# Optimization experiments

Hardware: AMD Instinct MI355X
Metric: run time of the kernel (lower is better)

## Reference

```python
import jax, jax.numpy as jnp
import numpy as np

N = 50000      # total nodes in batch
E = 800000     # edges (before self-loops)
F_IN = 64      # num_node_features
HID = 64       # hidden_channels
H = 4          # heads (hidden layers)
G = 512        # number of graphs
NEG_SLOPE = 0.2


def setup_inputs() -> dict:
    key = jax.random.key(0)
    ks = jax.random.split(key, 12)
    x = jax.random.normal(ks[0], (N, F_IN), dtype=jnp.float32)
    edge_index = jax.random.randint(ks[1], (2, E), 0, N, dtype=jnp.int32)
    # deterministic sorted graph assignment: all G segments non-empty
    batch = ((jnp.arange(N) * G) // N).astype(jnp.int32)

    def w(k, shape, fan_in):
        return (jax.random.normal(k, shape, jnp.float32) / np.sqrt(fan_in)).astype(jnp.float32)

    return {
        "x": x, "edge_index": edge_index, "batch": batch,
        # layer 0: in=F_IN, heads=4, concat -> out 256
        "W0": w(ks[2], (F_IN, H * HID), F_IN),
        "att_src0": w(ks[3], (H, HID), HID), "att_dst0": w(ks[4], (H, HID), HID),
        "b0": jnp.zeros((H * HID,), jnp.float32),
        # layer 1: in=256, heads=4, concat -> out 256
        "W1": w(ks[5], (H * HID, H * HID), H * HID),
        "att_src1": w(ks[6], (H, HID), HID), "att_dst1": w(ks[7], (H, HID), HID),
        "b1": jnp.zeros((H * HID,), jnp.float32),
        # layer 2: in=256, heads=1, concat=False -> out 64
        "W2": w(ks[8], (H * HID, 1 * HID), H * HID),
        "att_src2": w(ks[9], (1, HID), HID), "att_dst2": w(ks[10], (1, HID), HID),
        "b2": jnp.zeros((HID,), jnp.float32),
    }


def gat_layer(x, src, dst, W, att_src, att_dst, bias, concat):
    # PyG GATConv (eval mode, add_self_loops already applied to src/dst)
    n = x.shape[0]
    h, c = att_src.shape
    z = (x @ W).reshape(n, h, c)                       # [N,H,C]
    a_s = jnp.sum(z * att_src, axis=-1)                # [N,H]
    a_d = jnp.sum(z * att_dst, axis=-1)                # [N,H]
    e = jax.nn.leaky_relu(a_s[src] + a_d[dst], NEG_SLOPE)   # [E',H]
    # segment softmax over incoming edges of each target node
    e_max = jax.ops.segment_max(e, dst, num_segments=n)
    e_exp = jnp.exp(e - e_max[dst])
    denom = jax.ops.segment_sum(e_exp, dst, num_segments=n)
    alpha = e_exp / (denom[dst] + 1e-16)               # [E',H]
    msg = z[src] * alpha[:, :, None]                   # [E',H,C]
    out = jax.ops.segment_sum(msg, dst, num_segments=n)  # [N,H,C]
    out = out.reshape(n, h * c) if concat else out.mean(axis=1)
    return out + bias


def reference(x, edge_index, batch, W0, att_src0, att_dst0, b0,
              W1, att_src1, att_dst1, b1, W2, att_src2, att_dst2, b2):
    n = x.shape[0]
    loops = jnp.arange(n, dtype=edge_index.dtype)
    src = jnp.concatenate([edge_index[0], loops])
    dst = jnp.concatenate([edge_index[1], loops])
    h = gat_layer(x, src, dst, W0, att_src0, att_dst0, b0, concat=True)
    h = jax.nn.elu(h)
    h = gat_layer(h, src, dst, W1, att_src1, att_dst1, b1, concat=True)
    h = jax.nn.elu(h)
    h = gat_layer(h, src, dst, W2, att_src2, att_dst2, b2, concat=False)
    # global max pool over nodes of each graph -> [G, HID]
    return jax.ops.segment_max(h, batch, num_segments=G)
```

## Files before the change

### kernel.cpp

```cpp
#include <hip/hip_runtime.h>
#include <math.h>


typedef __attribute__((ext_vector_type(8))) short short8v;
typedef __attribute__((ext_vector_type(16))) float f32x16;

__device__ __forceinline__ float lrelu(float x) { return x > 0.f ? x : 0.2f * x; }

__device__ __forceinline__ unsigned short f2bf(float x) {
    unsigned u = __float_as_uint(x);
    return (unsigned short)((u + 0x7FFFu + ((u >> 16) & 1u)) >> 16);
}
__device__ __forceinline__ float bf2f(unsigned short h) {
    return __uint_as_float(((unsigned)h) << 16);
}
__device__ __forceinline__ float readlane_f(float v, int l) {
    return __uint_as_float((unsigned)__builtin_amdgcn_readlane((int)__float_as_uint(v), l));
}

__global__ void k_count(const int* __restrict__ dst, int E, int* __restrict__ deg) {
    int e = blockIdx.x * 256 + threadIdx.x;
    if (e < E) atomicAdd(&deg[dst[e]], 1);
}

__global__ __launch_bounds__(256) void k_scan1(const int* __restrict__ deg,
                                               int* __restrict__ incl,
                                               int* __restrict__ bsum, int N) {
    const int i = blockIdx.x * 256 + threadIdx.x;
    const int lane = threadIdx.x & 63;
    const int wv = threadIdx.x >> 6;
    int sc = (i < N) ? deg[i] + 1 : 0;
#pragma unroll
    for (int off = 1; off < 64; off <<= 1) {
        int t = __shfl_up(sc, off, 64);
        if (lane >= off) sc += t;
    }
    __shared__ int wsum[4];
    if (lane == 63) wsum[wv] = sc;
    __syncthreads();
    int woff = 0;
#pragma unroll
    for (int k = 0; k < 3; k++)
        if (wv > k) woff += wsum[k];
    sc += woff;
    if (i < N) incl[i] = sc;
    if (threadIdx.x == 255) bsum[blockIdx.x] = sc;
}

__global__ __launch_bounds__(1024) void k_scan2(int* __restrict__ bsum, int nb) {
    const int t = threadIdx.x;
    const int lane = t & 63;
    const int wv = t >> 6;
    int sc = (t < nb) ? bsum[t] : 0;
#pragma unroll
    for (int off = 1; off < 64; off <<= 1) {
        int u = __shfl_up(sc, off, 64);
        if (lane >= off) sc += u;
    }
    __shared__ int wsum[16];
    if (lane == 63) wsum[wv] = sc;
    __syncthreads();
    int woff = 0;
#pragma unroll
    for (int k = 0; k < 15; k++)
        if (wv > k) woff += wsum[k];
    sc += woff;
    if (t < nb) bsum[t] = sc;
}

__global__ void k_scan3(const int* __restrict__ deg, const int* __restrict__ incl,
                        const int* __restrict__ bsum, int* __restrict__ rowptr,
                        int* __restrict__ cursor, int N, int nb) {
    int i = blockIdx.x * 256 + threadIdx.x;
    if (i < N) {
        const int off = (blockIdx.x > 0) ? bsum[blockIdx.x - 1] : 0;
        const int excl = incl[i] + off - (deg[i] + 1);
        rowptr[i] = excl;
        cursor[i] = excl;
        if (i == N - 1) rowptr[N] = bsum[nb - 1];
    }
}

__global__ void k_scatter(const int* __restrict__ src, const int* __restrict__ dst, int E,
                          int N, int* __restrict__ cursor, int* __restrict__ col) {
    int e = blockIdx.x * 256 + threadIdx.x;
    if (e < E) {
        int d = dst[e];
        int p = atomicAdd(&cursor[d], 1);
        col[p] = src[e];
    } else if (e < E + N) {
        int n = e - E;
        int p = atomicAdd(&cursor[n], 1);
        col[p] = n;
    }
}

__global__ void k_setup(const float* __restrict__ W0, const float* __restrict__ W1,
                        const float* __restrict__ W2, const float* __restrict__ as0,
                        const float* __restrict__ ad0,
                        unsigned short* __restrict__ wt0h, unsigned short* __restrict__ wt0l,
                        unsigned short* __restrict__ wt1h, unsigned short* __restrict__ wt1l,
                        unsigned short* __restrict__ wt2h, unsigned short* __restrict__ wt2l,
                        float* __restrict__ vs0, float* __restrict__ vd0) {
    const int b = blockIdx.x;
    const int t = threadIdx.x;
    if (b < 64) {
        const int i = b * 256 + t;
        const int c = i / 64, k = i % 64;
        const float xw = W0[(size_t)k * 256 + c];
        const unsigned short h = f2bf(xw);
        wt0h[i] = h;
        wt0l[i] = f2bf(xw - bf2f(h));
    } else if (b < 320) {
        const int i = (b - 64) * 256 + t;
        const int c = i / 256, k = i % 256;
        const float xw = W1[(size_t)k * 256 + c];
        const unsigned short h = f2bf(xw);
        wt1h[i] = h;
        wt1l[i] = f2bf(xw - bf2f(h));
    } else if (b < 384) {
        const int i = (b - 320) * 256 + t;
        const int c = i / 256, k = i % 256;
        const float xw = W2[(size_t)k * 64 + c];
        const unsigned short h = f2bf(xw);
        wt2h[i] = h;
        wt2l[i] = f2bf(xw - bf2f(h));
    } else {
        const int k = t;
        if (k < 64) {
            for (int h = 0; h < 4; h++) {
                float s = 0.f, d = 0.f;
                for (int c = 0; c < 64; c++) {
                    float w = W0[(size_t)k * 256 + h * 64 + c];
                    s = fmaf(w, as0[h * 64 + c], s);
                    d = fmaf(w, ad0[h * 64 + c], d);
                }
                vs0[h * 64 + k] = s;
                vd0[h * 64 + k] = d;
            }
        }
    }
}

__global__ __launch_bounds__(256) void k_att0(
    const float* __restrict__ X, const float* __restrict__ vs, const float* __restrict__ vd,
    float* __restrict__ As, float* __restrict__ Ad, unsigned short* __restrict__ xb, int N) {
    const int n = blockIdx.x * 4 + (threadIdx.x >> 6);
    const int lane = threadIdx.x & 63;
    if (n >= N) return;
    const float xv = X[(size_t)n * 64 + lane];
    xb[(size_t)n * 64 + lane] = f2bf(xv);
#pragma unroll
    for (int h = 0; h < 4; h++) {
        float ps = xv * vs[h * 64 + lane];
        float pd = xv * vd[h * 64 + lane];
#pragma unroll
        for (int off = 1; off < 64; off <<= 1) {
            ps += __shfl_xor(ps, off, 64);
            pd += __shfl_xor(pd, off, 64);
        }
        if (lane == 0) {
            As[(size_t)n * 4 + h] = ps;
            Ad[(size_t)n * 4 + h] = pd;
        }
    }
}

__global__ __launch_bounds__(256) void k_aggx(
    const unsigned short* __restrict__ Xb, const float* __restrict__ As,
    const float* __restrict__ Ad, const int* __restrict__ rowptr,
    const int* __restrict__ col, unsigned short* __restrict__ ohi,
    unsigned short* __restrict__ olo, int N) {
    __shared__ float wlds[4][64][4];
    const int wv = threadIdx.x >> 6;
    const int n = blockIdx.x * 4 + wv;
    const int lane = threadIdx.x & 63;
    if (n >= N) return;

    const int start = rowptr[n];
    const int total = rowptr[n + 1] - start;
    const int* __restrict__ cp = col + start;
    const float4 adn = *reinterpret_cast<const float4*>(Ad + (size_t)n * 4);

    float a0 = 0.f, a1 = 0.f, a2 = 0.f, a3 = 0.f;
    float4 dv = make_float4(0.f, 0.f, 0.f, 0.f);

    for (int base = 0; base < total; base += 64) {
        const int cnt = min(64, total - base);
        const int i = base + lane;
        int s = 0;
        float4 w = make_float4(0.f, 0.f, 0.f, 0.f);
        if (i < total) {
            s = cp[i];
            const float4 av = *reinterpret_cast<const float4*>(As + (size_t)s * 4);
            w.x = __expf(lrelu(av.x + adn.x));
            w.y = __expf(lrelu(av.y + adn.y));
            w.z = __expf(lrelu(av.z + adn.z));
            w.w = __expf(lrelu(av.w + adn.w));
        }
        dv.x += w.x; dv.y += w.y; dv.z += w.z; dv.w += w.w;
        *reinterpret_cast<float4*>(&wlds[wv][lane][0]) = w;

        int jj = 0;
        for (; jj + 4 <= cnt; jj += 4) {
            int sb[4];
            float4 wj[4];
            float xv[4];
#pragma unroll
            for (int u = 0; u < 4; u++) {
                sb[u] = __builtin_amdgcn_readlane(s, jj + u);
                wj[u] = *reinterpret_cast<const float4*>(&wlds[wv][jj + u][0]);
            }
#pragma unroll
            for (int u = 0; u < 4; u++) xv[u] = bf2f(Xb[(size_t)sb[u] * 64 + lane]);
#pragma unroll
            for (int u = 0; u < 4; u++) {
                a0 = fmaf(wj[u].x, xv[u], a0);
                a1 = fmaf(wj[u].y, xv[u], a1);
                a2 = fmaf(wj[u].z, xv[u], a2);
                a3 = fmaf(wj[u].w, xv[u], a3);
            }
        }
        for (; jj < cnt; jj++) {
            const int s0 = __builtin_amdgcn_readlane(s, jj);
            const float4 wj = *reinterpret_cast<const float4*>(&wlds[wv][jj][0]);
            const float xv = bf2f(Xb[(size_t)s0 * 64 + lane]);
            a0 = fmaf(wj.x, xv, a0);
            a1 = fmaf(wj.y, xv, a1);
            a2 = fmaf(wj.z, xv, a2);
            a3 = fmaf(wj.w, xv, a3);
        }
    }

#pragma unroll
    for (int off = 1; off < 64; off <<= 1) {
        dv.x += __shfl_xor(dv.x, off, 64);
        dv.y += __shfl_xor(dv.y, off, 64);
        dv.z += __shfl_xor(dv.z, off, 64);
        dv.w += __shfl_xor(dv.w, off, 64);
    }

    const float o[4] = {a0 / (dv.x + 1e-16f), a1 / (dv.y + 1e-16f),
                        a2 / (dv.z + 1e-16f), a3 / (dv.w + 1e-16f)};
#pragma unroll
    for (int h = 0; h < 4; h++) {
        const unsigned short hb = f2bf(o[h]);
        ohi[(size_t)n * 256 + h * 64 + lane] = hb;
        olo[(size_t)n * 256 + h * 64 + lane] = f2bf(o[h] - bf2f(hb));
    }
}

__global__ __launch_bounds__(256) void k_gemm_pe(
    const unsigned short* __restrict__ Ahi, const unsigned short* __restrict__ Alo,
    const unsigned short* __restrict__ Bhi, const unsigned short* __restrict__ Blo,
    const float* __restrict__ bias, unsigned short* __restrict__ Ohi, int N) {
    constexpr int LD = 40, BM = 128, K = 64;
    __shared__ unsigned short sa[2][BM * LD];
    __shared__ unsigned short sb[2][64 * LD];

    const int tid = threadIdx.x;
    const int n0 = blockIdx.x * BM;
    const int hh = blockIdx.y;
    const int wid = tid >> 6, lane = tid & 63;

    const unsigned short* __restrict__ Ah = Ahi + hh * 64;
    const unsigned short* __restrict__ Al = Alo + hh * 64;
    const unsigned short* __restrict__ Bh = Bhi + hh * 64 * K;
    const unsigned short* __restrict__ Bl = Blo + hh * 64 * K;

    f32x16 acc[2];
#pragma unroll
    for (int n = 0; n < 2; n++)
#pragma unroll
        for (int i = 0; i < 16; i++) acc[n][i] = 0.f;

    const int srow = tid >> 2, schk = tid & 3;

    for (int kb = 0; kb < K; kb += 32) {
        __syncthreads();
#pragma unroll
        for (int rr = 0; rr < 2; rr++) {
            const int r = srow + rr * 64;
            const int row = n0 + r;
            short8v vh = {0, 0, 0, 0, 0, 0, 0, 0}, vl = {0, 0, 0, 0, 0, 0, 0, 0};
            if (row < N) {
                vh = *reinterpret_cast<const short8v*>(Ah + (size_t)row * 256 + kb + schk * 8);
                vl = *reinterpret_cast<const short8v*>(Al + (size_t)row * 256 + kb + schk * 8);
            }
            *reinterpret_cast<short8v*>(&sa[0][r * LD + schk * 8]) = vh;
            *reinterpret_cast<short8v*>(&sa[1][r * LD + schk * 8]) = vl;
        }
        {
            const short8v vh =
                *reinterpret_cast<const short8v*>(Bh + (size_t)srow * K + kb + schk * 8);
            const short8v vl =
                *reinterpret_cast<const short8v*>(Bl + (size_t)srow * K + kb + schk * 8);
            *reinterpret_cast<short8v*>(&sb[0][srow * LD + schk * 8]) = vh;
            *reinterpret_cast<short8v*>(&sb[1][srow * LD + schk * 8]) = vl;
        }
        __syncthreads();
#pragma unroll
        for (int ks = 0; ks < 2; ks++) {
            const int koff = ks * 16 + (lane >> 5) * 8;
            const int ar = wid * 32 + (lane & 31);
            const short8v ah = *reinterpret_cast<const short8v*>(&sa[0][ar * LD + koff]);
            const short8v al = *reinterpret_cast<const short8v*>(&sa[1][ar * LD + koff]);
            short8v bh[2], bl[2];
#pragma unroll
            for (int n = 0; n < 2; n++) {
                const int br = n * 32 + (lane & 31);
                bh[n] = *reinterpret_cast<const short8v*>(&sb[0][br * LD + koff]);
                bl[n] = *reinterpret_cast<const short8v*>(&sb[1][br * LD + koff]);
            }
#pragma unroll
            for (int n = 0; n < 2; n++) {
                acc[n] = __builtin_amdgcn_mfma_f32_32x32x16_bf16(ah, bh[n], acc[n], 0, 0, 0);
                acc[n] = __builtin_amdgcn_mfma_f32_32x32x16_bf16(ah, bl[n], acc[n], 0, 0, 0);
                acc[n] = __builtin_amdgcn_mfma_f32_32x32x16_bf16(al, bh[n], acc[n], 0, 0, 0);
            }
        }
    }

    const int rowb = n0 + wid * 32 + 4 * (lane >> 5);
#pragma unroll
    for (int n = 0; n < 2; n++) {
        const int c = (lane & 31) + n * 32;
        const float bv = bias[hh * 64 + c];
#pragma unroll
        for (int r = 0; r < 16; r++) {
            const int row = rowb + (r & 3) + 8 * (r >> 2);
            if (row < N) {
                float ov = acc[n][r] + bv;
                ov = (ov > 0.f) ? ov : expm1f(ov);
                Ohi[(size_t)row * 256 + hh * 64 + c] = f2bf(ov);
            }
        }
    }
}

template <int K, int COLS, int BM, int BN, int WN, int OUTMODE>
__global__ __launch_bounds__(256) void k_gemm_z(
    const unsigned short* __restrict__ Ahi,
    const unsigned short* __restrict__ Bhi, const unsigned short* __restrict__ Blo,
    const float* __restrict__ att_src, const float* __restrict__ att_dst,
    unsigned short* __restrict__ Zb, unsigned char* __restrict__ Zq,
    float* __restrict__ scq, float* __restrict__ As, float* __restrict__ Ad, int N) {
    constexpr int LD = 40;
    constexpr int WAVES_N = BN / WN;
    constexpr int WAVES_M = 4 / WAVES_N;
    constexpr int WM = BM / WAVES_M;
    constexpr int MW = WM / 32, NW = WN / 32;
    constexpr int H = COLS / 64;
    __shared__ unsigned short sa[BM * LD];
    __shared__ unsigned short sb[2][BN * LD];

    const int tid = threadIdx.x;
    const int n0 = blockIdx.x * BM;
    const int c0 = blockIdx.y * BN;
    const int wid = tid >> 6, lane = tid & 63;
    const int wr = wid / WAVES_N, wc = wid % WAVES_N;

    f32x16 acc[MW][NW];
#pragma unroll
    for (int m = 0; m < MW; m++)
#pragma unroll
        for (int n = 0; n < NW; n++)
#pragma unroll
            for (int i = 0; i < 16; i++) acc[m][n][i] = 0.f;

    const int srow = tid >> 2, schk = tid & 3;

    for (int kb = 0; kb < K; kb += 32) {
        __syncthreads();
#pragma unroll
        for (int rr = 0; rr < BM / 64; rr++) {
            const int r = srow + rr * 64;
            const int row = n0 + r;
            short8v vh = {0, 0, 0, 0, 0, 0, 0, 0};
            if (row < N)
                vh = *reinterpret_cast<const short8v*>(Ahi + (size_t)row * K + kb + schk * 8);
            *reinterpret_cast<short8v*>(&sa[r * LD + schk * 8]) = vh;
        }
#pragma unroll
        for (int rr = 0; rr < BN / 64; rr++) {
            const int cc = srow + rr * 64;
            const short8v vh =
                *reinterpret_cast<const short8v*>(Bhi + (size_t)(c0 + cc) * K + kb + schk * 8);
            const short8v vl =
                *reinterpret_cast<const short8v*>(Blo + (size_t)(c0 + cc) * K + kb + schk * 8);
            *reinterpret_cast<short8v*>(&sb[0][cc * LD + schk * 8]) = vh;
            *reinterpret_cast<short8v*>(&sb[1][cc * LD + schk * 8]) = vl;
        }
        __syncthreads();
#pragma unroll
        for (int ks = 0; ks < 2; ks++) {
            const int koff = ks * 16 + (lane >> 5) * 8;
            short8v ah[MW], bh[NW], bl[NW];
#pragma unroll
            for (int m = 0; m < MW; m++) {
                const int ar = wr * WM + m * 32 + (lane & 31);
                ah[m] = *reinterpret_cast<const short8v*>(&sa[ar * LD + koff]);
            }
#pragma unroll
            for (int n = 0; n < NW; n++) {
                const int br = wc * WN + n * 32 + (lane & 31);
                bh[n] = *reinterpret_cast<const short8v*>(&sb[0][br * LD + koff]);
                bl[n] = *reinterpret_cast<const short8v*>(&sb[1][br * LD + koff]);
            }
#pragma unroll
            for (int m = 0; m < MW; m++)
#pragma unroll
                for (int n = 0; n < NW; n++) {
                    acc[m][n] = __builtin_amdgcn_mfma_f32_32x32x16_bf16(ah[m], bh[n], acc[m][n], 0, 0, 0);
                    acc[m][n] = __builtin_amdgcn_mfma_f32_32x32x16_bf16(ah[m], bl[n], acc[m][n], 0, 0, 0);
                }
        }
    }

    const int colb = c0 + wc * WN + (lane & 31);
    const int rowb = n0 + wr * WM + 4 * (lane >> 5);

    if constexpr (OUTMODE == 0) {
#pragma unroll
        for (int m = 0; m < MW; m++)
#pragma unroll
            for (int n = 0; n < NW; n++)
#pragma unroll
                for (int r = 0; r < 16; r++) {
                    const int row = rowb + m * 32 + (r & 3) + 8 * (r >> 2);
                    if (row < N) Zb[(size_t)row * COLS + colb + n * 32] = f2bf(acc[m][n][r]);
                }
    } else {
        float lmax = 0.f;
#pragma unroll
        for (int m = 0; m < MW; m++)
#pragma unroll
            for (int n = 0; n < NW; n++)
#pragma unroll
                for (int r = 0; r < 16; r++) lmax = fmaxf(lmax, fabsf(acc[m][n][r]));
#pragma unroll
        for (int off = 1; off < 64; off <<= 1) lmax = fmaxf(lmax, __shfl_xor(lmax, off, 64));
        __shared__ float smax[4];
        if (lane == 0) smax[wid] = lmax;
        __syncthreads();
        const float qmax = fmaxf(fmaxf(smax[wc], smax[wc + 2]), 1e-20f);
        const float sc = qmax * (1.f / 127.f);
        const float rsc = 127.f / qmax;
        if (lane == 0 && wr == 0) scq[blockIdx.x * 4 + blockIdx.y * 2 + wc] = sc;
#pragma unroll
        for (int m = 0; m < MW; m++)
#pragma unroll
            for (int n = 0; n < NW; n++)
#pragma unroll
                for (int r = 0; r < 16; r++) {
                    const int row = rowb + m * 32 + (r & 3) + 8 * (r >> 2);
                    if (row < N) {
                        int q = __float2int_rn(acc[m][n][r] * rsc) + 128;
                        q = min(255, max(0, q));
                        Zq[(size_t)row * COLS + colb + n * 32] = (unsigned char)q;
                    }
                }
    }

    const int hh = (c0 + wc * WN) >> 6;
    float asv[NW], adv[NW];
#pragma unroll
    for (int n = 0; n < NW; n++) {
        asv[n] = att_src[colb + n * 32];
        adv[n] = att_dst[colb + n * 32];
    }
#pragma unroll
    for (int m = 0; m < MW; m++)
#pragma unroll
        for (int r = 0; r < 16; r++) {
            const int row = rowb + m * 32 + (r & 3) + 8 * (r >> 2);
            float ps = 0.f, pd = 0.f;
#pragma unroll
            for (int n = 0; n < NW; n++) {
                ps = fmaf(acc[m][n][r], asv[n], ps);
                pd = fmaf(acc[m][n][r], adv[n], pd);
            }
#pragma unroll
            for (int off = 1; off < 32; off <<= 1) {
                ps += __shfl_xor(ps, off, 64);
                pd += __shfl_xor(pd, off, 64);
            }
            if ((lane & 31) == 0 && row < N) {
                As[(size_t)row * H + hh] = ps;
                Ad[(size_t)row * H + hh] = pd;
            }
        }
}

__device__ __forceinline__ unsigned fenc(float f) {
    unsigned u = __float_as_uint(f);
    return (u & 0x80000000u) ? ~u : (u | 0x80000000u);
}

__global__ __launch_bounds__(256) void k_agg4(
    const unsigned char* __restrict__ Zq, const float* __restrict__ scq,
    const float* __restrict__ As, const float* __restrict__ Ad,
    const int* __restrict__ rowptr, const int* __restrict__ col,
    const float* __restrict__ bias, unsigned short* __restrict__ ohi, int N) {
    __shared__ float wlds[4][64][4];
    const int wv = threadIdx.x >> 6;
    const int n = blockIdx.x * 4 + wv;
    const int lane = threadIdx.x & 63;
    if (n >= N) return;
    const int h = lane >> 4;
    const int qidx = lane >> 4;

    const int start = rowptr[n];
    const int total = rowptr[n + 1] - start;
    const int* __restrict__ cp = col + start;
    const float4 adn = *reinterpret_cast<const float4*>(Ad + (size_t)n * 4);
    const unsigned char* __restrict__ Zl = Zq + lane * 4;

    float a0 = 0.f, a1 = 0.f, a2 = 0.f, a3 = 0.f;
    float corr = 0.f;
    float4 dv = make_float4(0.f, 0.f, 0.f, 0.f);

    for (int base = 0; base < total; base += 64) {
        const int cnt = min(64, total - base);
        const int i = base + lane;
        int s = 0;
        float4 w = make_float4(0.f, 0.f, 0.f, 0.f);
        if (i < total) {
            s = cp[i];
            const float4 av = *reinterpret_cast<const float4*>(As + (size_t)s * 4);
            w.x = __expf(lrelu(av.x + adn.x));
            w.y = __expf(lrelu(av.y + adn.y));
            w.z = __expf(lrelu(av.z + adn.z));
            w.w = __expf(lrelu(av.w + adn.w));
        }
        dv.x += w.x; dv.y += w.y; dv.z += w.z; dv.w += w.w;
        *reinterpret_cast<float4*>(&wlds[wv][lane][0]) = w;

        int jj = 0;
        for (; jj + 8 <= cnt; jj += 8) {
            int sb[8];
            float ws[8], scv[8];
            unsigned zb[8];
#pragma unroll
            for (int u = 0; u < 8; u++) {
                sb[u] = __builtin_amdgcn_readlane(s, jj + u);
                ws[u] = wlds[wv][jj + u][h];
            }
#pragma unroll
            for (int u = 0; u < 8; u++) {
                zb[u] = *reinterpret_cast<const unsigned*>(Zl + (size_t)sb[u] * 256);
                scv[u] = scq[(sb[u] >> 7) * 4 + qidx];
            }
#pragma unroll
            for (int u = 0; u < 8; u++) {
                const float wsc = ws[u] * scv[u];
                a0 = fmaf(wsc, (float)(zb[u] & 0xffu), a0);
                a1 = fmaf(wsc, (float)((zb[u] >> 8) & 0xffu), a1);
                a2 = fmaf(wsc, (float)((zb[u] >> 16) & 0xffu), a2);
                a3 = fmaf(wsc, (float)(zb[u] >> 24), a3);
                corr += wsc;
            }
        }
        for (; jj + 4 <= cnt; jj += 4) {
            int sb[4];
            float ws[4], scv[4];
            unsigned zb[4];
#pragma unroll
            for (int u = 0; u < 4; u++) {
                sb[u] = __builtin_amdgcn_readlane(s, jj + u);
                ws[u] = wlds[wv][jj + u][h];
            }
#pragma unroll
            for (int u = 0; u < 4; u++) {
                zb[u] = *reinterpret_cast<const unsigned*>(Zl + (size_t)sb[u] * 256);
                scv[u] = scq[(sb[u] >> 7) * 4 + qidx];
            }
#pragma unroll
            for (int u = 0; u < 4; u++) {
                const float wsc = ws[u] * scv[u];
                a0 = fmaf(wsc, (float)(zb[u] & 0xffu), a0);
                a1 = fmaf(wsc, (float)((zb[u] >> 8) & 0xffu), a1);
                a2 = fmaf(wsc, (float)((zb[u] >> 16) & 0xffu), a2);
                a3 = fmaf(wsc, (float)(zb[u] >> 24), a3);
                corr += wsc;
            }
        }
        for (; jj < cnt; jj++) {
            const int s0 = __builtin_amdgcn_readlane(s, jj);
            const float ws = wlds[wv][jj][h];
            const unsigned zb = *reinterpret_cast<const unsigned*>(Zl + (size_t)s0 * 256);
            const float wsc = ws * scq[(s0 >> 7) * 4 + qidx];
            a0 = fmaf(wsc, (float)(zb & 0xffu), a0);
            a1 = fmaf(wsc, (float)((zb >> 8) & 0xffu), a1);
            a2 = fmaf(wsc, (float)((zb >> 16) & 0xffu), a2);
            a3 = fmaf(wsc, (float)(zb >> 24), a3);
            corr += wsc;
        }
    }

    a0 -= 128.f * corr;
    a1 -= 128.f * corr;
    a2 -= 128.f * corr;
    a3 -= 128.f * corr;

#pragma unroll
    for (int off = 1; off < 64; off <<= 1) {
        dv.x += __shfl_xor(dv.x, off, 64);
        dv.y += __shfl_xor(dv.y, off, 64);
        dv.z += __shfl_xor(dv.z, off, 64);
        dv.w += __shfl_xor(dv.w, off, 64);
    }
    const float den = (h == 0) ? dv.x : (h == 1) ? dv.y : (h == 2) ? dv.z : dv.w;
    const float inv = 1.f / (den + 1e-16f);
    float o[4] = {a0, a1, a2, a3};
#pragma unroll
    for (int j = 0; j < 4; j++) {
        float ov = o[j] * inv + bias[lane * 4 + j];
        o[j] = (ov > 0.f) ? ov : expm1f(ov);
    }
    const ushort4 vh = make_ushort4(f2bf(o[0]), f2bf(o[1]), f2bf(o[2]), f2bf(o[3]));
    *reinterpret_cast<ushort4*>(ohi + (size_t)n * 256 + lane * 4) = vh;
}

__global__ __launch_bounds__(256) void k_agg1(
    const unsigned short* __restrict__ Zb, const float* __restrict__ As,
    const float* __restrict__ Ad, const int* __restrict__ rowptr,
    const int* __restrict__ col, const float* __restrict__ bias,
    const int* __restrict__ batch, unsigned* __restrict__ enc, int N) {
    const int n = blockIdx.x * 4 + (threadIdx.x >> 6);
    const int lane = threadIdx.x & 63;
    if (n >= N) return;

    const int start = rowptr[n];
    const int total = rowptr[n + 1] - start;
    const int* __restrict__ cp = col + start;
    const float adn = Ad[n];

    float acc = 0.f, denom = 0.f;

    for (int base = 0; base < total; base += 64) {
        const int cnt = min(64, total - base);
        const int i = base + lane;
        int s = 0;
        float w = 0.f;
        if (i < total) {
            s = cp[i];
            w = __expf(lrelu(As[s] + adn));
        }
        denom += w;

        int jj = 0;
        for (; jj + 8 <= cnt; jj += 8) {
            int sb[8];
            float wb[8], zb[8];
#pragma unroll
            for (int u = 0; u < 8; u++) {
                sb[u] = __builtin_amdgcn_readlane(s, jj + u);
                wb[u] = readlane_f(w, jj + u);
            }
#pragma unroll
            for (int u = 0; u < 8; u++) zb[u] = bf2f(Zb[(size_t)sb[u] * 64 + lane]);
#pragma unroll
            for (int u = 0; u < 8; u++) acc = fmaf(wb[u], zb[u], acc);
        }
        for (; jj < cnt; jj++) {
            const int s0 = __builtin_amdgcn_readlane(s, jj);
            const float w0 = readlane_f(w, jj);
            acc = fmaf(w0, bf2f(Zb[(size_t)s0 * 64 + lane]), acc);
        }
    }

#pragma unroll
    for (int off = 1; off < 64; off <<= 1) denom += __shfl_xor(denom, off, 64);

    const float ov = acc / (denom + 1e-16f) + bias[lane];
    const int g = batch[n];
    atomicMax(&enc[g * 64 + lane], fenc(ov));
}

__global__ void k_decode(const unsigned* __restrict__ enc, float* __restrict__ out, int M) {
    int id = blockIdx.x * 256 + threadIdx.x;
    if (id < M) {
        unsigned e = enc[id];
        unsigned u = (e & 0x80000000u) ? (e & 0x7FFFFFFFu) : ~e;
        out[id] = __uint_as_float(u);
    }
}

extern "C" void kernel_launch(void* const* d_in, const int* in_sizes, int n_in,
                              void* d_out, int out_size, void* d_ws, size_t ws_size,
                              hipStream_t stream) {
    const float* x = (const float*)d_in[0];
    const int* edge_index = (const int*)d_in[1];
    const int* batch = (const int*)d_in[2];
    const float* W0 = (const float*)d_in[3];
    const float* as0 = (const float*)d_in[4];
    const float* ad0 = (const float*)d_in[5];
    const float* b0 = (const float*)d_in[6];
    const float* W1 = (const float*)d_in[7];
    const float* as1 = (const float*)d_in[8];
    const float* ad1 = (const float*)d_in[9];
    const float* b1 = (const float*)d_in[10];
    const float* W2 = (const float*)d_in[11];
    const float* as2 = (const float*)d_in[12];
    const float* ad2 = (const float*)d_in[13];
    const float* b2 = (const float*)d_in[14];

    const int N = in_sizes[0] / 64;
    const int E = in_sizes[1] / 2;
    const int G = out_size / 64;
    const int Et = E + N;

    const int* srcs = edge_index;
    const int* dsts = edge_index + E;

    char* p = (char*)d_ws;
    auto alloc = [&](size_t bytes) {
        void* r = (void*)p;
        p += (bytes + 255) & ~(size_t)255;
        return r;
    };
    unsigned short* Zb = (unsigned short*)alloc((size_t)N * 64 * 2);
    unsigned char* Zq = (unsigned char*)alloc((size_t)N * 256);
    unsigned short* Hb = (unsigned short*)alloc((size_t)N * 256 * 2);
    unsigned short* xb = (unsigned short*)alloc((size_t)N * 64 * 2);
    unsigned short* Axhi = (unsigned short*)alloc((size_t)N * 256 * 2);
    unsigned short* Axlo = (unsigned short*)alloc((size_t)N * 256 * 2);
    float* As = (float*)alloc((size_t)N * 4 * 4);
    float* Ad = (float*)alloc((size_t)N * 4 * 4);
    int* deg = (int*)alloc((size_t)N * 4);
    int* incl = (int*)alloc((size_t)N * 4);
    int* bsum = (int*)alloc(1024 * 4);
    int* rowptr = (int*)alloc((size_t)(N + 1) * 4);
    int* cursor = (int*)alloc((size_t)N * 4);
    int* col = (int*)alloc((size_t)Et * 4);
    unsigned short* wt0h = (unsigned short*)alloc(256 * 64 * 2);
    unsigned short* wt0l = (unsigned short*)alloc(256 * 64 * 2);
    unsigned short* wt1h = (unsigned short*)alloc(256 * 256 * 2);
    unsigned short* wt1l = (unsigned short*)alloc(256 * 256 * 2);
    unsigned short* wt2h = (unsigned short*)alloc(64 * 256 * 2);
    unsigned short* wt2l = (unsigned short*)alloc(64 * 256 * 2);
    float* vs0 = (float*)alloc(4 * 64 * 4);
    float* vd0 = (float*)alloc(4 * 64 * 4);
    const int gm = (N + 127) / 128;
    float* scq = (float*)alloc((size_t)gm * 4 * 4);
    unsigned* enc = (unsigned*)alloc((size_t)G * 64 * 4);

    hipMemsetAsync(deg, 0, (size_t)N * 4, stream);
    hipMemsetAsync(enc, 0, (size_t)G * 64 * 4, stream);

    const int eb = (E + 255) / 256;
    const int nb = (N + 255) / 256;
    const int ab = (N + 3) / 4;

    k_count<<<eb, 256, 0, stream>>>(dsts, E, deg);
    k_scan1<<<nb, 256, 0, stream>>>(deg, incl, bsum, N);
    k_scan2<<<1, 1024, 0, stream>>>(bsum, nb);
    k_scan3<<<nb, 256, 0, stream>>>(deg, incl, bsum, rowptr, cursor, N, nb);
    k_scatter<<<(Et + 255) / 256, 256, 0, stream>>>(srcs, dsts, E, N, cursor, col);

    k_setup<<<385, 256, 0, stream>>>(W0, W1, W2, as0, ad0, wt0h, wt0l, wt1h, wt1l,
                                     wt2h, wt2l, vs0, vd0);

    k_att0<<<ab, 256, 0, stream>>>(x, vs0, vd0, As, Ad, xb, N);
    k_aggx<<<ab, 256, 0, stream>>>(xb, As, Ad, rowptr, col, Axhi, Axlo, N);
    k_gemm_pe<<<dim3(gm, 4), 256, 0, stream>>>(Axhi, Axlo, wt0h, wt0l, b0, Hb, N);

    k_gemm_z<256, 256, 128, 128, 64, 1><<<dim3(gm, 2), 256, 0, stream>>>(
        Hb, wt1h, wt1l, as1, ad1, nullptr, Zq, scq, As, Ad, N);
    k_agg4<<<ab, 256, 0, stream>>>(Zq, scq, As, Ad, rowptr, col, b1, Hb, N);

    k_gemm_z<256, 64, 128, 64, 64, 0><<<dim3(gm, 1), 256, 0, stream>>>(
        Hb, wt2h, wt2l, as2, ad2, Zb, nullptr, nullptr, As, Ad, N);
    k_agg1<<<ab, 256, 0, stream>>>(Zb, As, Ad, rowptr, col, b2, batch, enc, N);
    k_decode<<<(G * 64 + 255) / 256, 256, 0, stream>>>(enc, (float*)d_out, G * 64);
}
```

Before: 378.1 us.

## Build CSR via two-pass bucketed radix scatter to localize atomics

Replaces the direct per-edge atomic scatter into the CSR column array with a two-level scheme. First, edges are grouped into 64-node destination buckets using block-local shared-memory histograms and a bucket prefix scan. Then a placement pass does the per-node atomics on records that are already clustered by destination. The aim is to turn random global atomics and writes into more local ones, at the cost of an extra 8-byte-per-edge intermediate buffer and an extra kernel. Self-loops are now counted in the histogram instead of being added in the scan. The bucket table is sized at 1024, which assumes N ≤ 65536.

```diff
diff --git a/kernel.cpp b/kernel.cpp
--- a/kernel.cpp
+++ b/kernel.cpp
@@ -4,6 +4,8 @@
 
 typedef __attribute__((ext_vector_type(8))) short short8v;
 typedef __attribute__((ext_vector_type(16))) float f32x16;
+
+constexpr int CH = 4096;
 
 __device__ __forceinline__ float lrelu(float x) { return x > 0.f ? x : 0.2f * x; }
 
@@ -18,9 +20,24 @@
     return __uint_as_float((unsigned)__builtin_amdgcn_readlane((int)__float_as_uint(v), l));
 }
 
-__global__ void k_count(const int* __restrict__ dst, int E, int* __restrict__ deg) {
-    int e = blockIdx.x * 256 + threadIdx.x;
-    if (e < E) atomicAdd(&deg[dst[e]], 1);
+__global__ __launch_bounds__(256) void k_hist(const int* __restrict__ dst, int E, int N,
+                                              int* __restrict__ deg, int* __restrict__ bcnt) {
+    __shared__ int h[1024];
+    for (int b = threadIdx.x; b < 1024; b += 256) h[b] = 0;
+    __syncthreads();
+    const int base = blockIdx.x * CH;
+    const int Et = E + N;
+    for (int i = threadIdx.x; i < CH; i += 256) {
+        const int e = base + i;
+        if (e < Et) {
+            const int d = (e < E) ? dst[e] : (e - E);
+            atomicAdd(&deg[d], 1);
+            atomicAdd(&h[d >> 6], 1);
+        }
+    }
+    __syncthreads();
+    for (int b = threadIdx.x; b < 1024; b += 256)
+        if (h[b]) atomicAdd(&bcnt[b], h[b]);
 }
 
 __global__ __launch_bounds__(256) void k_scan1(const int* __restrict__ deg,
@@ -29,7 +46,7 @@
     const int i = blockIdx.x * 256 + threadIdx.x;
     const int lane = threadIdx.x & 63;
     const int wv = threadIdx.x >> 6;
-    int sc = (i < N) ? deg[i] + 1 : 0;
+    int sc = (i < N) ? deg[i] : 0;
 #pragma unroll
     for (int off = 1; off < 64; off <<= 1) {
         int t = __shfl_up(sc, off, 64);
@@ -47,11 +64,18 @@
     if (threadIdx.x == 255) bsum[blockIdx.x] = sc;
 }
 
-__global__ __launch_bounds__(1024) void k_scan2(int* __restrict__ bsum, int nb) {
+__global__ __launch_bounds__(1024) void k_scan2(int* __restrict__ bsum, int nb,
+                                                const int* __restrict__ bcnt,
+                                                int* __restrict__ bbase,
+                                                int* __restrict__ bcur, int nbk) {
     const int t = threadIdx.x;
     const int lane = t & 63;
     const int wv = t >> 6;
-    int sc = (t < nb) ? bsum[t] : 0;
+    const bool nodeScan = (blockIdx.x == 0);
+    const int cnt = nodeScan ? nb : nbk;
+    int v = 0;
+    if (t < cnt) v = nodeScan ? bsum[t] : bcnt[t];
+    int sc = v;
 #pragma unroll
     for (int off = 1; off < 64; off <<= 1) {
         int u = __shfl_up(sc, off, 64);
@@ -65,7 +89,14 @@
     for (int k = 0; k < 15; k++)
         if (wv > k) woff += wsum[k];
     sc += woff;
-    if (t < nb) bsum[t] = sc;
+    if (t < cnt) {
+        if (nodeScan) {
+            bsum[t] = sc;
+        } else {
+            bbase[t] = sc - v;
+            bcur[t] = sc - v;
+        }
+    }
 }
 
 __global__ void k_scan3(const int* __restrict__ deg, const int* __restrict__ incl,
@@ -74,24 +105,60 @@
     int i = blockIdx.x * 256 + threadIdx.x;
     if (i < N) {
         const int off = (blockIdx.x > 0) ? bsum[blockIdx.x - 1] : 0;
-        const int excl = incl[i] + off - (deg[i] + 1);
+        const int excl = incl[i] + off - deg[i];
         rowptr[i] = excl;
         cursor[i] = excl;
         if (i == N - 1) rowptr[N] = bsum[nb - 1];
     }
 }
 
-__global__ void k_scatter(const int* __restrict__ src, const int* __restrict__ dst, int E,
-                          int N, int* __restrict__ cursor, int* __restrict__ col) {
+__global__ __launch_bounds__(256) void k_bucket(const int* __restrict__ src,
+                                                const int* __restrict__ dst, int E, int N,
+                                                int* __restrict__ bcur,
+                                                uint2* __restrict__ rec) {
+    __shared__ int h[1024];
+    __shared__ int boff[1024];
+    for (int b = threadIdx.x; b < 1024; b += 256) h[b] = 0;
+    __syncthreads();
+    const int base = blockIdx.x * CH;
+    const int Et = E + N;
+    for (int i = threadIdx.x; i < CH; i += 256) {
+        const int e = base + i;
+        if (e < Et) {
+            const int d = (e < E) ? dst[e] : (e - E);
+            atomicAdd(&h[d >> 6], 1);
+        }
+    }
+    __syncthreads();
+    for (int b = threadIdx.x; b < 1024; b += 256)
+        boff[b] = h[b] ? atomicAdd(&bcur[b], h[b]) : 0;
+    __syncthreads();
+    for (int b = threadIdx.x; b < 1024; b += 256) h[b] = 0;
+    __syncthreads();
+    for (int i = threadIdx.x; i < CH; i += 256) {
+        const int e = base + i;
+        if (e < Et) {
+            int d, s;
+            if (e < E) {
+                d = dst[e];
+                s = src[e];
+            } else {
+                d = e - E;
+                s = d;
+            }
+            const int r = atomicAdd(&h[d >> 6], 1);
+            rec[boff[d >> 6] + r] = make_uint2((unsigned)s, (unsigned)d);
+        }
+    }
+}
+
+__global__ void k_place(const uint2* __restrict__ rec, int Et, int* __restrict__ cursor,
+                        int* __restrict__ col) {
     int e = blockIdx.x * 256 + threadIdx.x;
-    if (e < E) {
-        int d = dst[e];
-        int p = atomicAdd(&cursor[d], 1);
-        col[p] = src[e];
-    } else if (e < E + N) {
-        int n = e - E;
-        int p = atomicAdd(&cursor[n], 1);
-        col[p] = n;
+    if (e < Et) {
+        const uint2 rd = rec[e];
+        const int p = atomicAdd(&cursor[(int)rd.y], 1);
+        col[p] = (int)rd.x;
     }
 }
 
@@ -710,6 +777,7 @@
     const int E = in_sizes[1] / 2;
     const int G = out_size / 64;
     const int Et = E + N;
+    const int nbk = (N + 63) >> 6;
 
     const int* srcs = edge_index;
     const int* dsts = edge_index + E;
@@ -734,6 +802,10 @@
     int* rowptr = (int*)alloc((size_t)(N + 1) * 4);
     int* cursor = (int*)alloc((size_t)N * 4);
     int* col = (int*)alloc((size_t)Et * 4);
+    uint2* rec = (uint2*)alloc((size_t)Et * 8);
+    int* bcnt = (int*)alloc(1024 * 4);
+    int* bbase = (int*)alloc(1024 * 4);
+    int* bcur = (int*)alloc(1024 * 4);
     unsigned short* wt0h = (unsigned short*)alloc(256 * 64 * 2);
     unsigned short* wt0l = (unsigned short*)alloc(256 * 64 * 2);
     unsigned short* wt1h = (unsigned short*)alloc(256 * 256 * 2);
@@ -747,17 +819,19 @@
     unsigned* enc = (unsigned*)alloc((size_t)G * 64 * 4);
 
     hipMemsetAsync(deg, 0, (size_t)N * 4, stream);
+    hipMemsetAsync(bcnt, 0, 1024 * 4, stream);
     hipMemsetAsync(enc, 0, (size_t)G * 64 * 4, stream);
 
-    const int eb = (E + 255) / 256;
     const int nb = (N + 255) / 256;
     const int ab = (N + 3) / 4;
-
-    k_count<<<eb, 256, 0, stream>>>(dsts, E, deg);
+    const int hb = (Et + CH - 1) / CH;
+
+    k_hist<<<hb, 256, 0, stream>>>(dsts, E, N, deg, bcnt);
     k_scan1<<<nb, 256, 0, stream>>>(deg, incl, bsum, N);
-    k_scan2<<<1, 1024, 0, stream>>>(bsum, nb);
+    k_scan2<<<2, 1024, 0, stream>>>(bsum, nb, bcnt, bbase, bcur, nbk);
     k_scan3<<<nb, 256, 0, stream>>>(deg, incl, bsum, rowptr, cursor, N, nb);
-    k_scatter<<<(Et + 255) / 256, 256, 0, stream>>>(srcs, dsts, E, N, cursor, col);
+    k_bucket<<<hb, 256, 0, stream>>>(srcs, dsts, E, N, bcur, rec);
+    k_place<<<(Et + 255) / 256, 256, 0, stream>>>(rec, Et, cursor, col);
 
     k_setup<<<385, 256, 0, stream>>>(W0, W1, W2, as0, ad0, wt0h, wt0l, wt1h, wt1l,
                                      wt2h, wt2l, vs0, vd0);
```

New measurement: 362.2 us. -4.2%, faster.
